# Kernel optimization log

Hardware: AMD Instinct MI355X
Metric: run time of the kernel (lower is better)

## Reference

```python
import jax, jax.numpy as jnp
import numpy as np

NEG_SLOPE = 0.01  # torch F.leaky_relu default


def _mlp_block(x, mask, W, b):
    # x: [B,P,V,F]; mask: [B,P,V] bool; W: [H,F]; b: [H]
    h = jax.nn.leaky_relu(jnp.einsum('bpvf,hf->bpvh', x, W) + b, NEG_SLOPE)
    m = mask[..., None]
    out = jnp.where(m, h, 0.0)                                   # zeros at masked-out slots
    neg = jnp.where(m, out, -jnp.inf)
    pool = jnp.max(neg, axis=2, keepdims=True)                   # [B,P,1,H] masked max-pool
    any_valid = jnp.any(mask, axis=2)[:, :, None, None]
    pool = jnp.where(any_valid, pool, 0.0)                       # fully-masked polylines -> 0
    rep = jnp.broadcast_to(pool, out.shape)
    return jnp.concatenate([out, rep], axis=-1)                  # [B,P,V,2H]


def setup_inputs() -> dict:
    key = jax.random.key(0)
    ks = jax.random.split(key, 8)
    B, P, V, F, H = 32, 512, 32, 16, 64
    input_var = jax.random.normal(ks[0], (B, P, V, F), dtype=jnp.float32)
    input_mask = jax.random.bernoulli(ks[1], 0.8, (B, P, V))
    s = 1.0 / np.sqrt(F)
    W1 = jax.random.uniform(ks[2], (H, F), jnp.float32, -s, s)
    b1 = jax.random.uniform(ks[3], (H,), jnp.float32, -s, s)
    s2 = 1.0 / np.sqrt(2 * H)
    W2 = jax.random.uniform(ks[4], (H, 2 * H), jnp.float32, -s2, s2)
    b2 = jax.random.uniform(ks[5], (H,), jnp.float32, -s2, s2)
    W3 = jax.random.uniform(ks[6], (H, 2 * H), jnp.float32, -s2, s2)
    b3 = jax.random.uniform(ks[7], (H,), jnp.float32, -s2, s2)
    return {"input_var": input_var, "input_mask": input_mask,
            "W1": W1, "b1": b1, "W2": W2, "b2": b2, "W3": W3, "b3": b3,
            "size1": P, "size2": V}


def reference(input_var, input_mask, W1, b1, W2, b2, W3, b3, size1, size2):
    hidden = W1.shape[0]
    x = _mlp_block(input_var, input_mask, W1, b1)
    y = _mlp_block(x, input_mask, W2, b2)
    z = _mlp_block(y, input_mask, W3, b3)
    out = z[:, :, 0, -hidden:]                                   # pooled half, same across V
    out = jnp.where(jnp.any(input_mask, axis=2)[..., None], out, 0.0)
    return out
```

## Files before the change

### kernel.cpp

```cpp
#include <hip/hip_runtime.h>
#include <math.h>

namespace {
constexpr int kXS = 72;
constexpr float kSlope = 0.01f;

typedef short bf16x8 __attribute__((ext_vector_type(8)));
typedef float f32x4  __attribute__((ext_vector_type(4)));

__device__ __forceinline__ float lrelu(float x) { return fmaxf(x, kSlope * x); }

__device__ __forceinline__ unsigned short bfrne(float a) {
    union { float f; unsigned u; } v; v.f = a;
    return (unsigned short)((v.u + 0x7FFFu + ((v.u >> 16) & 1u)) >> 16);
}

__global__ void prep_weights(const float* __restrict__ W1,
                             const float* __restrict__ W2,
                             const float* __restrict__ W3,
                             unsigned short* __restrict__ ws)
{
    int t = blockIdx.x * blockDim.x + threadIdx.x;
    if (t >= 36 * 64) return;
    int f = t >> 6, l = t & 63, c = l & 15, q = l >> 4;
    unsigned short v[8] = {0, 0, 0, 0, 0, 0, 0, 0};
    const float* src = nullptr; int row = 0, k0 = 0, K = 0;
    if (f < 4) {
        if (q < 2) { src = W1; row = 16 * f + c; k0 = q * 8; K = 16; }
    } else if (f < 20) {
        int g = f - 4;  src = W2; row = 16 * (g >> 2) + c; k0 = (g & 3) * 32 + q * 8; K = 128;
    } else {
        int g = f - 20; src = W3; row = 16 * (g >> 2) + c; k0 = (g & 3) * 32 + q * 8; K = 128;
    }
    if (src) {
        #pragma unroll
        for (int j = 0; j < 8; ++j) v[j] = bfrne(src[row * K + k0 + j]);
    }
    unsigned short* dst = ws + (size_t)f * 512 + l * 8;
    *(ushort4*)(dst)     = make_ushort4(v[0], v[1], v[2], v[3]);
    *(ushort4*)(dst + 4) = make_ushort4(v[4], v[5], v[6], v[7]);
}

__global__ __launch_bounds__(256, 4) void fused_mlp_v7(
    const float* __restrict__ X, const int* __restrict__ M,
    const unsigned short* __restrict__ WF,
    const float* __restrict__ B1, const float* __restrict__ B2,
    const float* __restrict__ B3, float* __restrict__ OUT)
{
    __shared__ __align__(16) short sX[4][32 * kXS];
    __shared__ __align__(16) short sP[4][64];

    const int t = threadIdx.x, w = t >> 6, l = t & 63, c = l & 15, q = l >> 4;
    const size_t bp = (size_t)blockIdx.x * 4 + w;

    short* xb = &sX[w][0];
    short* pl = &sP[w][0];

    float4 xr[2][2];
    if (q < 2) {
        #pragma unroll
        for (int mt = 0; mt < 2; ++mt) {
            const float4* p = (const float4*)(X + (bp * 32 + 16 * mt + c) * 16 + q * 8);
            xr[mt][0] = p[0]; xr[mt][1] = p[1];
        }
    }
    const int4* Mp = (const int4*)(M + bp * 32);
    const int4 mr0 = Mp[q], mr1 = Mp[4 + q];
    const unsigned mbits =
        (mr0.x ? 1u : 0u)  | (mr0.y ? 2u : 0u)  | (mr0.z ? 4u : 0u)  | (mr0.w ? 8u : 0u) |
        (mr1.x ? 16u : 0u) | (mr1.y ? 32u : 0u) | (mr1.z ? 64u : 0u) | (mr1.w ? 128u : 0u);
    const bool anyv = __any(mbits != 0);

    f32x4 acc[2][4];

    {
        bf16x8 a1f[2];
        #pragma unroll
        for (int mt = 0; mt < 2; ++mt) {
            bf16x8 v = {};
            if (q < 2) {
                float4 f0 = xr[mt][0], f1 = xr[mt][1];
                v[0] = (short)bfrne(f0.x); v[1] = (short)bfrne(f0.y);
                v[2] = (short)bfrne(f0.z); v[3] = (short)bfrne(f0.w);
                v[4] = (short)bfrne(f1.x); v[5] = (short)bfrne(f1.y);
                v[6] = (short)bfrne(f1.z); v[7] = (short)bfrne(f1.w);
            }
            a1f[mt] = v;
        }
        #pragma unroll
        for (int nt = 0; nt < 4; ++nt) {
            float b = B1[16 * nt + c];
            bf16x8 wf = *(const bf16x8*)(WF + (size_t)nt * 512 + l * 8);
            f32x4 c0 = { b, b, b, b };
            acc[0][nt] = __builtin_amdgcn_mfma_f32_16x16x32_bf16(a1f[0], wf, c0, 0, 0, 0);
            acc[1][nt] = __builtin_amdgcn_mfma_f32_16x16x32_bf16(a1f[1], wf, c0, 0, 0, 0);
        }
    }

    auto epilogue = [&]() {
        float pool[4];
        #pragma unroll
        for (int nt = 0; nt < 4; ++nt) {
            float pv = -INFINITY;
            #pragma unroll
            for (int mt = 0; mt < 2; ++mt) {
                short* base = &xb[(16 * mt + 4 * q) * kXS + 16 * nt + c];
                #pragma unroll
                for (int r = 0; r < 4; ++r) {
                    float y = lrelu(acc[mt][nt][r]);
                    bool mk = (mbits >> (mt * 4 + r)) & 1;
                    float o = mk ? y : 0.f;
                    pv = mk ? fmaxf(pv, y) : pv;
                    base[r * kXS] = (short)bfrne(o);
                }
            }
            pv = fmaxf(pv, __shfl_xor(pv, 16));
            pv = fmaxf(pv, __shfl_xor(pv, 32));
            pool[nt] = anyv ? pv : 0.f;
        }
        float ps = (q & 2) ? ((q & 1) ? pool[3] : pool[2])
                           : ((q & 1) ? pool[1] : pool[0]);
        pl[16 * q + c] = (short)bfrne(ps);
    };

    auto layerK = [&](int fb, const float* __restrict__ Bv) {
        bf16x8 a00 = *(const bf16x8*)&xb[(     c) * kXS      + q * 8];
        bf16x8 a01 = *(const bf16x8*)&xb[(16 + c) * kXS      + q * 8];
        bf16x8 a10 = *(const bf16x8*)&xb[(     c) * kXS + 32 + q * 8];
        bf16x8 a11 = *(const bf16x8*)&xb[(16 + c) * kXS + 32 + q * 8];
        bf16x8 ap0 = *(const bf16x8*)&pl[q * 8];
        bf16x8 ap1 = *(const bf16x8*)&pl[32 + q * 8];
        #pragma unroll
        for (int nt = 0; nt < 4; ++nt) {
            float b = Bv[16 * nt + c];
            acc[0][nt] = f32x4{ b, b, b, b };
            acc[1][nt] = acc[0][nt];
        }
        #pragma unroll
        for (int ks = 0; ks < 4; ++ks) {
            bf16x8 am0 = (ks == 0) ? a00 : (ks == 1) ? a10 : (ks == 2) ? ap0 : ap1;
            bf16x8 am1 = (ks == 0) ? a01 : (ks == 1) ? a11 : (ks == 2) ? ap0 : ap1;
            #pragma unroll
            for (int nt = 0; nt < 4; ++nt) {
                bf16x8 wf = *(const bf16x8*)(WF + ((size_t)(fb + nt * 4 + ks)) * 512 + l * 8);
                acc[0][nt] = __builtin_amdgcn_mfma_f32_16x16x32_bf16(am0, wf, acc[0][nt], 0, 0, 0);
                acc[1][nt] = __builtin_amdgcn_mfma_f32_16x16x32_bf16(am1, wf, acc[1][nt], 0, 0, 0);
            }
        }
    };

    epilogue();
    layerK(4, B2);
    epilogue();
    layerK(20, B3);

    {
        float pool[4];
        #pragma unroll
        for (int nt = 0; nt < 4; ++nt) {
            float pv = -INFINITY;
            #pragma unroll
            for (int mt = 0; mt < 2; ++mt)
                #pragma unroll
                for (int r = 0; r < 4; ++r) {
                    bool mk = (mbits >> (mt * 4 + r)) & 1;
                    float y = lrelu(acc[mt][nt][r]);
                    pv = mk ? fmaxf(pv, y) : pv;
                }
            pv = fmaxf(pv, __shfl_xor(pv, 16));
            pv = fmaxf(pv, __shfl_xor(pv, 32));
            pool[nt] = anyv ? pv : 0.f;
        }
        float ps = (q & 2) ? ((q & 1) ? pool[3] : pool[2])
                           : ((q & 1) ? pool[1] : pool[0]);
        OUT[bp * 64 + 16 * q + c] = ps;
    }
}
}

extern "C" void kernel_launch(void* const* d_in, const int* in_sizes, int n_in,
                              void* d_out, int out_size, void* d_ws, size_t ws_size,
                              hipStream_t stream) {
    (void)in_sizes; (void)n_in; (void)ws_size; (void)out_size;
    const float* X  = (const float*)d_in[0];
    const int*   M  = (const int*)d_in[1];
    const float* W1 = (const float*)d_in[2];
    const float* B1 = (const float*)d_in[3];
    const float* W2 = (const float*)d_in[4];
    const float* B2 = (const float*)d_in[5];
    const float* W3 = (const float*)d_in[6];
    const float* B3 = (const float*)d_in[7];
    float* OUT = (float*)d_out;
    unsigned short* WF = (unsigned short*)d_ws;

    prep_weights<<<(36 * 64 + 255) / 256, 256, 0, stream>>>(W1, W2, W3, WF);
    fused_mlp_v7<<<4096, 256, 0, stream>>>(X, M, WF, B1, B2, B3, OUT);
}
```

Baseline: 120.0 us.

## Split each polyline across two waves by output-column halves

Each polyline now gets a 128-thread block instead of one wave. The two waves each compute half of the 64 hidden columns and share the activations through LDS with block barriers. This halves accumulator registers per wave and doubles the number of waves, aiming for more latency hiding. In exchange, both waves load and convert the same input and mask, three __syncthreads are added per block, and MFMA work per wave gets smaller.

```diff
diff --git a/kernel.cpp b/kernel.cpp
--- a/kernel.cpp
+++ b/kernel.cpp
@@ -41,20 +41,18 @@
     *(ushort4*)(dst + 4) = make_ushort4(v[4], v[5], v[6], v[7]);
 }
 
-__global__ __launch_bounds__(256, 4) void fused_mlp_v7(
+__global__ __launch_bounds__(128, 6) void fused_mlp_v8(
     const float* __restrict__ X, const int* __restrict__ M,
     const unsigned short* __restrict__ WF,
     const float* __restrict__ B1, const float* __restrict__ B2,
     const float* __restrict__ B3, float* __restrict__ OUT)
 {
-    __shared__ __align__(16) short sX[4][32 * kXS];
-    __shared__ __align__(16) short sP[4][64];
+    __shared__ __align__(16) short xb[32 * kXS];
+    __shared__ __align__(16) short pl[64];
 
-    const int t = threadIdx.x, w = t >> 6, l = t & 63, c = l & 15, q = l >> 4;
-    const size_t bp = (size_t)blockIdx.x * 4 + w;
-
-    short* xb = &sX[w][0];
-    short* pl = &sP[w][0];
+    const int t = threadIdx.x, u = t >> 6, l = t & 63, c = l & 15, q = l >> 4;
+    const size_t bp = (size_t)blockIdx.x;
+    const int nb = 32 * u;
 
     float4 xr[2][2];
     if (q < 2) {
@@ -71,7 +69,7 @@
         (mr1.x ? 16u : 0u) | (mr1.y ? 32u : 0u) | (mr1.z ? 64u : 0u) | (mr1.w ? 128u : 0u);
     const bool anyv = __any(mbits != 0);
 
-    f32x4 acc[2][4];
+    f32x4 acc[2][2];
 
     {
         bf16x8 a1f[2];
@@ -88,9 +86,9 @@
             a1f[mt] = v;
         }
         #pragma unroll
-        for (int nt = 0; nt < 4; ++nt) {
-            float b = B1[16 * nt + c];
-            bf16x8 wf = *(const bf16x8*)(WF + (size_t)nt * 512 + l * 8);
+        for (int nt = 0; nt < 2; ++nt) {
+            float b = B1[nb + 16 * nt + c];
+            bf16x8 wf = *(const bf16x8*)(WF + (size_t)(2 * u + nt) * 512 + l * 8);
             f32x4 c0 = { b, b, b, b };
             acc[0][nt] = __builtin_amdgcn_mfma_f32_16x16x32_bf16(a1f[0], wf, c0, 0, 0, 0);
             acc[1][nt] = __builtin_amdgcn_mfma_f32_16x16x32_bf16(a1f[1], wf, c0, 0, 0, 0);
@@ -98,13 +96,13 @@
     }
 
     auto epilogue = [&]() {
-        float pool[4];
+        float pool[2];
         #pragma unroll
-        for (int nt = 0; nt < 4; ++nt) {
+        for (int nt = 0; nt < 2; ++nt) {
             float pv = -INFINITY;
             #pragma unroll
             for (int mt = 0; mt < 2; ++mt) {
-                short* base = &xb[(16 * mt + 4 * q) * kXS + 16 * nt + c];
+                short* base = &xb[(16 * mt + 4 * q) * kXS + nb + 16 * nt + c];
                 #pragma unroll
                 for (int r = 0; r < 4; ++r) {
                     float y = lrelu(acc[mt][nt][r]);
@@ -118,9 +116,7 @@
             pv = fmaxf(pv, __shfl_xor(pv, 32));
             pool[nt] = anyv ? pv : 0.f;
         }
-        float ps = (q & 2) ? ((q & 1) ? pool[3] : pool[2])
-                           : ((q & 1) ? pool[1] : pool[0]);
-        pl[16 * q + c] = (short)bfrne(ps);
+        if (q < 2) pl[nb + 16 * q + c] = (short)bfrne(q ? pool[1] : pool[0]);
     };
 
     auto layerK = [&](int fb, const float* __restrict__ Bv) {
@@ -131,8 +127,8 @@
         bf16x8 ap0 = *(const bf16x8*)&pl[q * 8];
         bf16x8 ap1 = *(const bf16x8*)&pl[32 + q * 8];
         #pragma unroll
-        for (int nt = 0; nt < 4; ++nt) {
-            float b = Bv[16 * nt + c];
+        for (int nt = 0; nt < 2; ++nt) {
+            float b = Bv[nb + 16 * nt + c];
             acc[0][nt] = f32x4{ b, b, b, b };
             acc[1][nt] = acc[0][nt];
         }
@@ -141,8 +137,9 @@
             bf16x8 am0 = (ks == 0) ? a00 : (ks == 1) ? a10 : (ks == 2) ? ap0 : ap1;
             bf16x8 am1 = (ks == 0) ? a01 : (ks == 1) ? a11 : (ks == 2) ? ap0 : ap1;
             #pragma unroll
-            for (int nt = 0; nt < 4; ++nt) {
-                bf16x8 wf = *(const bf16x8*)(WF + ((size_t)(fb + nt * 4 + ks)) * 512 + l * 8);
+            for (int nt = 0; nt < 2; ++nt) {
+                int f = fb + (2 * u + nt) * 4 + ks;
+                bf16x8 wf = *(const bf16x8*)(WF + (size_t)f * 512 + l * 8);
                 acc[0][nt] = __builtin_amdgcn_mfma_f32_16x16x32_bf16(am0, wf, acc[0][nt], 0, 0, 0);
                 acc[1][nt] = __builtin_amdgcn_mfma_f32_16x16x32_bf16(am1, wf, acc[1][nt], 0, 0, 0);
             }
@@ -150,30 +147,28 @@
     };
 
     epilogue();
+    __syncthreads();
     layerK(4, B2);
+    __syncthreads();
     epilogue();
+    __syncthreads();
     layerK(20, B3);
 
-    {
-        float pool[4];
+    #pragma unroll
+    for (int nt = 0; nt < 2; ++nt) {
+        float pv = -INFINITY;
         #pragma unroll
-        for (int nt = 0; nt < 4; ++nt) {
-            float pv = -INFINITY;
+        for (int mt = 0; mt < 2; ++mt)
             #pragma unroll
-            for (int mt = 0; mt < 2; ++mt)
-                #pragma unroll
-                for (int r = 0; r < 4; ++r) {
-                    bool mk = (mbits >> (mt * 4 + r)) & 1;
-                    float y = lrelu(acc[mt][nt][r]);
-                    pv = mk ? fmaxf(pv, y) : pv;
-                }
-            pv = fmaxf(pv, __shfl_xor(pv, 16));
-            pv = fmaxf(pv, __shfl_xor(pv, 32));
-            pool[nt] = anyv ? pv : 0.f;
-        }
-        float ps = (q & 2) ? ((q & 1) ? pool[3] : pool[2])
-                           : ((q & 1) ? pool[1] : pool[0]);
-        OUT[bp * 64 + 16 * q + c] = ps;
+            for (int r = 0; r < 4; ++r) {
+                bool mk = (mbits >> (mt * 4 + r)) & 1;
+                float y = lrelu(acc[mt][nt][r]);
+                pv = mk ? fmaxf(pv, y) : pv;
+            }
+        pv = fmaxf(pv, __shfl_xor(pv, 16));
+        pv = fmaxf(pv, __shfl_xor(pv, 32));
+        pv = anyv ? pv : 0.f;
+        if (q == 0) OUT[bp * 64 + nb + 16 * nt + c] = pv;
     }
 }
 }
@@ -194,5 +189,5 @@
     unsigned short* WF = (unsigned short*)d_ws;
 
     prep_weights<<<(36 * 64 + 255) / 256, 256, 0, stream>>>(W1, W2, W3, WF);
-    fused_mlp_v7<<<4096, 256, 0, stream>>>(X, M, WF, B1, B2, B3, OUT);
+    fused_mlp_v8<<<16384, 128, 0, stream>>>(X, M, WF, B1, B2, B3, OUT);
 }
```

Result: no change. 122.0 us (+1.7%).
